# Optimization experiments

Hardware: AMD Instinct MI355X
Metric: run time of the kernel (lower is better)

The kernel has to match this reference:

```python
import jax, jax.numpy as jnp
import numpy as np

B, S, H = 4, 4096, 1024
I = 2048        # intermediate_size
E = 16          # num_experts
K = 2           # top_k


def setup_inputs() -> dict:
    key = jax.random.key(0)
    ks = jax.random.split(key, 5)
    scale = 0.02
    return {
        "hidden_states": jax.random.normal(ks[0], (B, S, H), dtype=jnp.float32),
        "w_gate": jax.random.normal(ks[1], (H, E), dtype=jnp.float32) * scale,
        "w_gate_proj": jax.random.normal(ks[2], (E, H, I), dtype=jnp.float32) * scale,
        "w_up_proj": jax.random.normal(ks[3], (E, H, I), dtype=jnp.float32) * scale,
        "w_down_proj": jax.random.normal(ks[4], (E, I, H), dtype=jnp.float32) * scale,
    }


def reference(hidden_states, w_gate, w_gate_proj, w_up_proj, w_down_proj):
    b, s, h = hidden_states.shape
    x = hidden_states.reshape(-1, h)                       # [T, H], T = b*s

    # --- gate: softmax router, top-k, renormalize (Mixtral-style) ---
    probs = jax.nn.softmax(x @ w_gate, axis=-1)            # [T, E]
    topk_vals, topk_idx = jax.lax.top_k(probs, K)          # [T, K]
    routing_weights = topk_vals / jnp.sum(topk_vals, axis=-1, keepdims=True)

    # --- per-expert SwiGLU FFN, combined via routing weights ---
    out = jnp.zeros_like(x)
    for e in range(E):
        # combined weight of expert e for each token (0 if not selected)
        we = jnp.sum(jnp.where(topk_idx == e, routing_weights, 0.0), axis=-1)  # [T]
        g = x @ w_gate_proj[e]                             # [T, I]
        u = x @ w_up_proj[e]                               # [T, I]
        y = (u * jax.nn.silu(g)) @ w_down_proj[e]          # [T, H]
        out = out + we[:, None] * y

    return out.reshape(b, s, h)
```

## Files before the change

kernel.cpp:

```cpp
#include <hip/hip_runtime.h>
#include <hip/hip_bf16.h>
#include <math.h>

#define T_TOK 16384
#define H_DIM 1024
#define I_DIM 2048
#define E_NUM 16
#define MAX_TILES 144

typedef short bf16x8 __attribute__((ext_vector_type(8)));
typedef float f32x4 __attribute__((ext_vector_type(4)));

static constexpr size_t XB_BYTES  = (size_t)T_TOK * H_DIM * 2;
static constexpr size_t WC_BYTES  = (size_t)E_NUM * 2 * I_DIM * H_DIM * 2;
static constexpr size_t WD_BYTES  = (size_t)E_NUM * H_DIM * I_DIM * 2;
static constexpr size_t HB_BYTES  = (size_t)2 * T_TOK * I_DIM * 2;
static constexpr size_t LIST_BYTES= (size_t)E_NUM * T_TOK * 4;

static constexpr size_t XB_OFF    = 0;
static constexpr size_t WC_OFF    = XB_OFF + XB_BYTES;
static constexpr size_t WDT_OFF   = WC_OFF + WC_BYTES;
static constexpr size_t HB_OFF    = WDT_OFF + WD_BYTES;
static constexpr size_t ROWS_OFF  = HB_OFF + HB_BYTES;
static constexpr size_t WTS_OFF   = ROWS_OFF + LIST_BYTES;
static constexpr size_t CNT_OFF   = WTS_OFF + LIST_BYTES;
static constexpr size_t BASE_OFF  = CNT_OFF + 256;
static constexpr size_t TILES_OFF = BASE_OFF + 256;
static constexpr size_t NT_OFF    = TILES_OFF + 2048;

__device__ __forceinline__ void async_ld16(void* lds, const void* g) {
    __builtin_amdgcn_global_load_lds(
        (const __attribute__((address_space(1))) void*)g,
        (__attribute__((address_space(3))) void*)lds,
        16, 0, 0);
}

__global__ void transpose_convert_kernel(const float* __restrict__ in,
                                         __hip_bfloat16* __restrict__ out,
                                         int R, int C, int Nd, int ioff) {
    __shared__ float tile[32][33];
    int e = blockIdx.z;
    int c0 = blockIdx.x * 32;
    int r0 = blockIdx.y * 32;
    const float* pin = in + (size_t)e * R * C;
    __hip_bfloat16* pout = out + (size_t)e * Nd * R;
    int tx = threadIdx.x, ty = threadIdx.y;
    #pragma unroll
    for (int j = 0; j < 4; j++)
        tile[ty + j*8][tx] = pin[(size_t)(r0 + ty + j*8) * C + (c0 + tx)];
    __syncthreads();
    #pragma unroll
    for (int j = 0; j < 4; j++) {
        int c = c0 + ty + j*8;
        int n = (ioff < 0) ? c : 32*(c >> 4) + ioff + (c & 15);
        pout[(size_t)n * R + (r0 + tx)] = __float2bfloat16(tile[tx][ty + j*8]);
    }
}

__global__ void router_kernel(const float* __restrict__ x, const float* __restrict__ wg,
                              int* __restrict__ cnt, int* __restrict__ rows,
                              float* __restrict__ wts, __hip_bfloat16* __restrict__ xb) {
    int t = blockIdx.x;
    int lane = threadIdx.x;
    float xv[16];
    const float* xp = x + (size_t)t * H_DIM;
    __hip_bfloat16* xbp = xb + (size_t)t * H_DIM;
    #pragma unroll
    for (int j = 0; j < 16; j++) xv[j] = xp[j*64 + lane];
    #pragma unroll
    for (int j = 0; j < 16; j++) xbp[j*64 + lane] = __float2bfloat16(xv[j]);
    double logits[E_NUM];
    #pragma unroll
    for (int e = 0; e < E_NUM; e++) {
        double p = 0.0;
        #pragma unroll
        for (int j = 0; j < 16; j++)
            p += (double)xv[j] * (double)wg[(j*64 + lane) * E_NUM + e];
        #pragma unroll
        for (int off = 32; off > 0; off >>= 1) p += __shfl_down(p, off);
        logits[e] = p;
    }
    if (lane == 0) {
        int i1 = 0; double v1 = logits[0];
        #pragma unroll
        for (int e = 1; e < E_NUM; e++) if (logits[e] > v1) { v1 = logits[e]; i1 = e; }
        int i2 = -1; double v2 = -1e300;
        #pragma unroll
        for (int e = 0; e < E_NUM; e++) if (e != i1 && logits[e] > v2) { v2 = logits[e]; i2 = e; }
        double w1 = 1.0 / (1.0 + exp(v2 - v1));
        float w1f = (float)w1, w2f = (float)(1.0 - w1);
        int s1 = atomicAdd(&cnt[i1], 1);
        rows[i1 * T_TOK + s1] = t; wts[i1 * T_TOK + s1] = w1f;
        int s2 = atomicAdd(&cnt[i2], 1);
        rows[i2 * T_TOK + s2] = t; wts[i2 * T_TOK + s2] = w2f;
    }
}

__global__ void schedule_kernel(const int* __restrict__ cnt, int* __restrict__ base,
                                int* __restrict__ tiles, int* __restrict__ ntiles) {
    int lane = threadIdx.x;
    int c = (lane < E_NUM) ? cnt[lane] : 0;
    int m = (c + 255) >> 8;
    int b = c, t = m;
    #pragma unroll
    for (int off = 1; off < 16; off <<= 1) {
        int vb = __shfl_up(b, off);
        int vt = __shfl_up(t, off);
        if ((lane & 15) >= off) { b += vb; t += vt; }
    }
    int bex = b - c, tex = t - m;
    if (lane < E_NUM) {
        base[lane] = bex;
        for (int i = 0; i < m; i++) tiles[tex + i] = (lane << 16) | i;
        if (lane == E_NUM - 1) ntiles[0] = tex + m;
    }
}

template<int MODE>
__global__ __launch_bounds__(512) void moe_gemm_kernel(
    const __hip_bfloat16* __restrict__ Abase,
    const __hip_bfloat16* __restrict__ Bw,
    void* __restrict__ Cout,
    const int* __restrict__ rows, const float* __restrict__ wts,
    const int* __restrict__ cnt, const int* __restrict__ base,
    const int* __restrict__ tiles, const int* __restrict__ ntiles,
    int Kd, int Nd)
{
    if ((int)blockIdx.y >= ntiles[0]) return;
    int td = tiles[blockIdx.y];
    int e = td >> 16, tile = td & 0xffff;
    int cnt_e = cnt[e], base_e = base[e];
    int cnt_local = cnt_e - tile * 256;
    int bn = blockIdx.x;
    const int* rows_e = rows + e * T_TOK;
    const __hip_bfloat16* Be = Bw + (size_t)e * Nd * Kd;

    __shared__ __align__(16) __hip_bfloat16 As[2][8][256][8];
    __shared__ __align__(16) __hip_bfloat16 Bs[2][8][256][8];

    int tid = threadIdx.x;
    int w = tid >> 6, lane = tid & 63;

    const __hip_bfloat16* aptr[4];
    const __hip_bfloat16* bptr[4];
    uint32_t loff[4];
    #pragma unroll
    for (int j = 0; j < 4; j++) {
        int u = w * 4 + j;
        int chunk = u >> 2, quarter = u & 3;
        int r = quarter * 64 + lane;
        int gr = tile * 256 + r;
        size_t arow;
        if (MODE == 2) {
            int rr = base_e + gr;
            if (rr > 2 * T_TOK - 1) rr = 2 * T_TOK - 1;
            arow = (size_t)rr;
        } else {
            arow = (size_t)((gr < cnt_e) ? rows_e[gr] : 0);
        }
        aptr[j] = Abase + arow * Kd + chunk * 8;
        bptr[j] = Be + (size_t)(bn * 256 + r) * Kd + chunk * 8;
        loff[j] = (uint32_t)(u * 1024);
    }

    int wm = w >> 2, wn = w & 3;
    int l16 = lane & 15, quad = lane >> 4;

    f32x4 acc[8][4];
    #pragma unroll
    for (int a = 0; a < 8; a++)
        #pragma unroll
        for (int b = 0; b < 4; b++) acc[a][b] = (f32x4){0.f, 0.f, 0.f, 0.f};

    char* AsB = (char*)&As[0][0][0][0];
    char* BsB = (char*)&Bs[0][0][0][0];

    #pragma unroll
    for (int j = 0; j < 4; j++) {
        async_ld16(AsB + loff[j], aptr[j]);
        async_ld16(BsB + loff[j], bptr[j]);
        aptr[j] += 64; bptr[j] += 64;
    }
    __syncthreads();

    int nk = Kd >> 6;
    int cur = 0;
    for (int k0 = 0; k0 < nk; ++k0) {
        if (k0 + 1 < nk) {
            int nxt = cur ^ 1;
            #pragma unroll
            for (int j = 0; j < 4; j++) {
                async_ld16(AsB + nxt * 32768 + loff[j], aptr[j]);
                async_ld16(BsB + nxt * 32768 + loff[j], bptr[j]);
                aptr[j] += 64; bptr[j] += 64;
            }
        }
        #pragma unroll
        for (int ks = 0; ks < 2; ks++) {
            bf16x8 af[8], bfr[4];
            #pragma unroll
            for (int nt = 0; nt < 4; nt++)
                bfr[nt] = *(const bf16x8*)&Bs[cur][ks*4 + quad][wn*64 + nt*16 + l16][0];
            #pragma unroll
            for (int mt = 0; mt < 8; mt++)
                af[mt] = *(const bf16x8*)&As[cur][ks*4 + quad][wm*128 + mt*16 + l16][0];
            #pragma unroll
            for (int mt = 0; mt < 8; mt++)
                #pragma unroll
                for (int nt = 0; nt < 4; nt++)
                    acc[mt][nt] = __builtin_amdgcn_mfma_f32_16x16x32_bf16(af[mt], bfr[nt], acc[mt][nt], 0, 0, 0);
        }
        __syncthreads();
        cur ^= 1;
    }

    #pragma unroll
    for (int mt = 0; mt < 8; mt++) {
        #pragma unroll
        for (int r = 0; r < 4; r++) {
            int row = wm*128 + mt*16 + quad*4 + r;
            if (row < cnt_local) {
                int gr = tile * 256 + row;
                if (MODE == 0) {
                    __hip_bfloat16* hp = (__hip_bfloat16*)Cout + (size_t)(base_e + gr) * I_DIM;
                    #pragma unroll
                    for (int p = 0; p < 2; p++) {
                        int icol = (bn*8 + wn*2 + p)*16 + l16;
                        float g = acc[mt][2*p][r];
                        float u = acc[mt][2*p+1][r];
                        hp[icol] = __float2bfloat16(u * (g / (1.f + expf(-g))));
                    }
                } else {
                    int token = rows_e[gr];
                    float wt = (wts + e * T_TOK)[gr];
                    float* op = (float*)Cout + (size_t)token * H_DIM + bn*256 + wn*64;
                    #pragma unroll
                    for (int nt = 0; nt < 4; nt++)
                        atomicAdd(op + nt*16 + l16, wt * acc[mt][nt][r]);
                }
            }
        }
    }
}

extern "C" void kernel_launch(void* const* d_in, const int* in_sizes, int n_in,
                              void* d_out, int out_size, void* d_ws, size_t ws_size,
                              hipStream_t stream) {
    const float* x   = (const float*)d_in[0];
    const float* wg  = (const float*)d_in[1];
    const float* wgp = (const float*)d_in[2];
    const float* wup = (const float*)d_in[3];
    const float* wdp = (const float*)d_in[4];
    float* out = (float*)d_out;
    char* ws = (char*)d_ws;

    __hip_bfloat16* xb   = (__hip_bfloat16*)(ws + XB_OFF);
    __hip_bfloat16* Wc   = (__hip_bfloat16*)(ws + WC_OFF);
    __hip_bfloat16* Wdt  = (__hip_bfloat16*)(ws + WDT_OFF);
    __hip_bfloat16* hbuf = (__hip_bfloat16*)(ws + HB_OFF);
    int*   rowsp  = (int*)(ws + ROWS_OFF);
    float* wtsp   = (float*)(ws + WTS_OFF);
    int*   cntp   = (int*)(ws + CNT_OFF);
    int*   basep  = (int*)(ws + BASE_OFF);
    int*   tilesp = (int*)(ws + TILES_OFF);
    int*   ntp    = (int*)(ws + NT_OFF);

    hipMemsetAsync(cntp, 0, 256, stream);
    hipMemsetAsync(out, 0, (size_t)out_size * sizeof(float), stream);

    transpose_convert_kernel<<<dim3(I_DIM/32, H_DIM/32, E_NUM), dim3(32, 8), 0, stream>>>(
        wgp, Wc, H_DIM, I_DIM, 2*I_DIM, 0);
    transpose_convert_kernel<<<dim3(I_DIM/32, H_DIM/32, E_NUM), dim3(32, 8), 0, stream>>>(
        wup, Wc, H_DIM, I_DIM, 2*I_DIM, 16);
    transpose_convert_kernel<<<dim3(H_DIM/32, I_DIM/32, E_NUM), dim3(32, 8), 0, stream>>>(
        wdp, Wdt, I_DIM, H_DIM, H_DIM, -1);
    router_kernel<<<T_TOK, 64, 0, stream>>>(x, wg, cntp, rowsp, wtsp, xb);
    schedule_kernel<<<1, 64, 0, stream>>>(cntp, basep, tilesp, ntp);

    moe_gemm_kernel<0><<<dim3(2*I_DIM/256, MAX_TILES), 512, 0, stream>>>(
        xb, Wc, hbuf, rowsp, wtsp, cntp, basep, tilesp, ntp, H_DIM, 2*I_DIM);
    moe_gemm_kernel<2><<<dim3(H_DIM/256, MAX_TILES), 512, 0, stream>>>(
        hbuf, Wdt, out, rowsp, wtsp, cntp, basep, tilesp, ntp, I_DIM, H_DIM);
}
```

Before: 1.781 ms.

## Split GEMM k-loop into barrier-fenced phases with staggered async loads and setprio

Rewrites the main MFMA loop of the grouped expert GEMM. Each k-step is split into four sub-phases of fragment loads plus MFMAs, separated by s_barrier and wrapped in s_setprio. Next-tile global-to-LDS loads are staggered across the phases, and explicit vmcnt waits replace the full __syncthreads. The aim is better overlap of global loads, LDS reads and MFMA work, and fewer full drains of outstanding loads. The cost is many more barriers per iteration and reliance on hand-counted vmcnt values, which is fragile if the compiler adds other memory operations.

```diff
diff --git a/kernel.cpp b/kernel.cpp
--- a/kernel.cpp
+++ b/kernel.cpp
@@ -34,6 +34,10 @@
         (__attribute__((address_space(3))) void*)lds,
         16, 0, 0);
 }
+
+#define SBAR()    asm volatile("s_barrier" ::: "memory")
+#define WAITVM4() asm volatile("s_waitcnt vmcnt(4)" ::: "memory")
+#define WAITVM0() asm volatile("s_waitcnt vmcnt(0)" ::: "memory")
 
 __global__ void transpose_convert_kernel(const float* __restrict__ in,
                                          __hip_bfloat16* __restrict__ out,
@@ -141,8 +145,8 @@
     int tid = threadIdx.x;
     int w = tid >> 6, lane = tid & 63;
 
-    const __hip_bfloat16* aptr[4];
-    const __hip_bfloat16* bptr[4];
+    const __hip_bfloat16* aB[4];
+    const __hip_bfloat16* bB[4];
     uint32_t loff[4];
     #pragma unroll
     for (int j = 0; j < 4; j++) {
@@ -158,8 +162,8 @@
         } else {
             arow = (size_t)((gr < cnt_e) ? rows_e[gr] : 0);
         }
-        aptr[j] = Abase + arow * Kd + chunk * 8;
-        bptr[j] = Be + (size_t)(bn * 256 + r) * Kd + chunk * 8;
+        aB[j] = Abase + arow * Kd + chunk * 8;
+        bB[j] = Be + (size_t)(bn * 256 + r) * Kd + chunk * 8;
         loff[j] = (uint32_t)(u * 1024);
     }
 
@@ -175,43 +179,87 @@
     char* AsB = (char*)&As[0][0][0][0];
     char* BsB = (char*)&Bs[0][0][0][0];
 
-    #pragma unroll
-    for (int j = 0; j < 4; j++) {
-        async_ld16(AsB + loff[j], aptr[j]);
-        async_ld16(BsB + loff[j], bptr[j]);
-        aptr[j] += 64; bptr[j] += 64;
-    }
-    __syncthreads();
+    auto ISSUE = [&](int t, int j) {
+        int d = (t & 1) * 32768;
+        async_ld16(AsB + d + loff[j], aB[j] + (size_t)t * 64);
+        async_ld16(BsB + d + loff[j], bB[j] + (size_t)t * 64);
+    };
 
     int nk = Kd >> 6;
-    int cur = 0;
-    for (int k0 = 0; k0 < nk; ++k0) {
-        if (k0 + 1 < nk) {
-            int nxt = cur ^ 1;
-            #pragma unroll
-            for (int j = 0; j < 4; j++) {
-                async_ld16(AsB + nxt * 32768 + loff[j], aptr[j]);
-                async_ld16(BsB + nxt * 32768 + loff[j], bptr[j]);
-                aptr[j] += 64; bptr[j] += 64;
-            }
-        }
-        #pragma unroll
-        for (int ks = 0; ks < 2; ks++) {
-            bf16x8 af[8], bfr[4];
+
+    #pragma unroll
+    for (int j = 0; j < 4; j++) ISSUE(0, j);
+    if (nk > 1) { ISSUE(1, 0); ISSUE(1, 1); WAITVM4(); }
+    else        { WAITVM0(); }
+    SBAR();
+
+    for (int t = 0; t < nk; ++t) {
+        const int d = t & 1;
+        bf16x8 bfr[4], af[4];
+
+        #pragma unroll
+        for (int nt = 0; nt < 4; nt++)
+            bfr[nt] = *(const bf16x8*)&Bs[d][quad][wn*64 + nt*16 + l16][0];
+        #pragma unroll
+        for (int mt = 0; mt < 4; mt++)
+            af[mt] = *(const bf16x8*)&As[d][quad][wm*128 + mt*16 + l16][0];
+        if (t + 1 < nk) ISSUE(t + 1, 2);
+        SBAR();
+        __builtin_amdgcn_s_setprio(1);
+        #pragma unroll
+        for (int mt = 0; mt < 4; mt++)
             #pragma unroll
             for (int nt = 0; nt < 4; nt++)
-                bfr[nt] = *(const bf16x8*)&Bs[cur][ks*4 + quad][wn*64 + nt*16 + l16][0];
+                acc[mt][nt] = __builtin_amdgcn_mfma_f32_16x16x32_bf16(af[mt], bfr[nt], acc[mt][nt], 0, 0, 0);
+        __builtin_amdgcn_s_setprio(0);
+        SBAR();
+
+        #pragma unroll
+        for (int mt = 0; mt < 4; mt++)
+            af[mt] = *(const bf16x8*)&As[d][quad][wm*128 + (mt+4)*16 + l16][0];
+        if (t + 1 < nk) ISSUE(t + 1, 3);
+        SBAR();
+        __builtin_amdgcn_s_setprio(1);
+        #pragma unroll
+        for (int mt = 0; mt < 4; mt++)
             #pragma unroll
-            for (int mt = 0; mt < 8; mt++)
-                af[mt] = *(const bf16x8*)&As[cur][ks*4 + quad][wm*128 + mt*16 + l16][0];
+            for (int nt = 0; nt < 4; nt++)
+                acc[mt+4][nt] = __builtin_amdgcn_mfma_f32_16x16x32_bf16(af[mt], bfr[nt], acc[mt+4][nt], 0, 0, 0);
+        __builtin_amdgcn_s_setprio(0);
+        SBAR();
+
+        #pragma unroll
+        for (int nt = 0; nt < 4; nt++)
+            bfr[nt] = *(const bf16x8*)&Bs[d][4 + quad][wn*64 + nt*16 + l16][0];
+        #pragma unroll
+        for (int mt = 0; mt < 4; mt++)
+            af[mt] = *(const bf16x8*)&As[d][4 + quad][wm*128 + mt*16 + l16][0];
+        SBAR();
+        __builtin_amdgcn_s_setprio(1);
+        #pragma unroll
+        for (int mt = 0; mt < 4; mt++)
             #pragma unroll
-            for (int mt = 0; mt < 8; mt++)
-                #pragma unroll
-                for (int nt = 0; nt < 4; nt++)
-                    acc[mt][nt] = __builtin_amdgcn_mfma_f32_16x16x32_bf16(af[mt], bfr[nt], acc[mt][nt], 0, 0, 0);
-        }
-        __syncthreads();
-        cur ^= 1;
+            for (int nt = 0; nt < 4; nt++)
+                acc[mt][nt] = __builtin_amdgcn_mfma_f32_16x16x32_bf16(af[mt], bfr[nt], acc[mt][nt], 0, 0, 0);
+        __builtin_amdgcn_s_setprio(0);
+        SBAR();
+
+        #pragma unroll
+        for (int mt = 0; mt < 4; mt++)
+            af[mt] = *(const bf16x8*)&As[d][4 + quad][wm*128 + (mt+4)*16 + l16][0];
+        SBAR();
+        __builtin_amdgcn_s_setprio(1);
+        #pragma unroll
+        for (int mt = 0; mt < 4; mt++)
+            #pragma unroll
+            for (int nt = 0; nt < 4; nt++)
+                acc[mt+4][nt] = __builtin_amdgcn_mfma_f32_16x16x32_bf16(af[mt], bfr[nt], acc[mt+4][nt], 0, 0, 0);
+        __builtin_amdgcn_s_setprio(0);
+
+        SBAR();
+        if (t + 2 < nk) { ISSUE(t + 2, 0); ISSUE(t + 2, 1); WAITVM4(); }
+        else if (t + 1 < nk) { WAITVM0(); }
+        SBAR();
     }
 
     #pragma unroll
```

Result: no change. 1.814 ms (+1.9%).
